# Performance work log

Hardware: AMD Instinct MI355X
Metric: run time of the kernel (lower is better)

The kernel has to match this reference:

```python
import jax, jax.numpy as jnp
import numpy as np

D = 1024          # model_dim
BD = D // 2       # bottleneck_dim
K = 64            # num_splats
B, S = 8, 2048


def setup_inputs() -> dict:
    key = jax.random.key(0)
    ks = jax.random.split(key, 12)
    sc = 0.02
    return {
        "token_embeddings": jax.random.normal(ks[0], (B, S, D), jnp.float32),
        "splat_influences": jax.random.uniform(ks[1], (B, S, K), jnp.float32),
        # encoder: Linear(D -> BD), stored [in, out]
        "enc_W": jax.random.normal(ks[2], (D, BD), jnp.float32) * sc,
        "enc_b": jnp.zeros((BD,), jnp.float32),
        # per-splat transforms: K x Linear(BD -> BD)
        "trans_W": jax.random.normal(ks[3], (K, BD, BD), jnp.float32) * sc,
        "trans_b": jnp.zeros((K, BD), jnp.float32),
        # decoder: Linear(BD -> D)
        "dec_W": jax.random.normal(ks[4], (BD, D), jnp.float32) * sc,
        "dec_b": jnp.zeros((D,), jnp.float32),
        # flow gate: Linear(D -> D) + sigmoid
        "gate_W": jax.random.normal(ks[5], (D, D), jnp.float32) * sc,
        "gate_b": jnp.zeros((D,), jnp.float32),
    }


def reference(token_embeddings, splat_influences, enc_W, enc_b,
              trans_W, trans_b, dec_W, dec_b, gate_W, gate_b):
    # gather: [B,K,S] @ [B,S,D] -> [B,K,D]
    influences_t = jnp.swapaxes(splat_influences, 1, 2)          # [B,K,S]
    gathered = jnp.einsum('bks,bsd->bkd', influences_t, token_embeddings)
    total = jnp.clip(influences_t.sum(axis=2, keepdims=True), 1e-8, None)  # [B,K,1]
    gathered = gathered / total
    # encoder (dropout inactive at eval)
    encoded = jax.nn.relu(gathered @ enc_W + enc_b)              # [B,K,BD]
    # per-splat transform as grouped matmul
    transformed = jnp.einsum('bkd,kde->bke', encoded, trans_W) + trans_b  # [B,K,BD]
    decoded = transformed @ dec_W + dec_b                        # [B,K,D]
    # scatter back to tokens: [B,S,K] @ [B,K,D]
    flow = jnp.einsum('bsk,bkd->bsd', splat_influences, decoded)
    gate = jax.nn.sigmoid(token_embeddings @ gate_W + gate_b)    # [B,S,D]
    return flow * gate
```

## Files before the change

kernel.cpp:

```cpp
#include <hip/hip_runtime.h>

#define BB 8
#define SS 2048
#define DD 1024
#define BDD 512
#define NSP 64

typedef __attribute__((ext_vector_type(8))) short bf16x8;
typedef __attribute__((ext_vector_type(4))) float f32x4;
typedef unsigned short u16;
typedef unsigned int u32;

__device__ __forceinline__ u16 f2bf(float f) {
  u32 u = __builtin_bit_cast(u32, f);
  u = u + 0x7fffu + ((u >> 16) & 1u);
  return (u16)(u >> 16);
}

__device__ __forceinline__ void gl_lds16(const void* g, void* l) {
  __builtin_amdgcn_global_load_lds((const __attribute__((address_space(1))) void*)g,
                                   (__attribute__((address_space(3))) void*)l,
                                   16, 0, 0);
}

__global__ void k_prep_tok(const float* __restrict__ tok, u16* __restrict__ tokbf,
                           u16* __restrict__ tokT) {
  __shared__ u16 tile[64][80];
  int C0 = blockIdx.x * 64;
  int R0 = blockIdx.y * 64;
  int b = R0 >> 11, s0 = R0 & 2047;
  int t = threadIdx.x;
  int lr = t >> 3, lc = (t & 7) * 8;
#pragma unroll
  for (int i = 0; i < 2; ++i) {
    int r = lr + i * 32;
    const float* src = tok + (size_t)(R0 + r) * DD + C0 + lc;
    float4 a = *(const float4*)src;
    float4 bq = *(const float4*)(src + 4);
    uint4 v;
    v.x = f2bf(a.x) | ((u32)f2bf(a.y) << 16);
    v.y = f2bf(a.z) | ((u32)f2bf(a.w) << 16);
    v.z = f2bf(bq.x) | ((u32)f2bf(bq.y) << 16);
    v.w = f2bf(bq.z) | ((u32)f2bf(bq.w) << 16);
    *(uint4*)(tokbf + (size_t)(R0 + r) * DD + C0 + lc) = v;
    *(uint4*)&tile[r][lc] = v;
  }
  __syncthreads();
  int sseg = (t & 7) * 8;
#pragma unroll
  for (int i = 0; i < 2; ++i) {
    int dcol = (t >> 3) + i * 32;
    u16 a0 = tile[sseg + 0][dcol], a1 = tile[sseg + 1][dcol];
    u16 a2 = tile[sseg + 2][dcol], a3 = tile[sseg + 3][dcol];
    u16 a4 = tile[sseg + 4][dcol], a5 = tile[sseg + 5][dcol];
    u16 a6 = tile[sseg + 6][dcol], a7 = tile[sseg + 7][dcol];
    uint4 v;
    v.x = a0 | ((u32)a1 << 16);
    v.y = a2 | ((u32)a3 << 16);
    v.z = a4 | ((u32)a5 << 16);
    v.w = a6 | ((u32)a7 << 16);
    *(uint4*)(tokT + (size_t)b * DD * SS + (size_t)(C0 + dcol) * SS + s0 + sseg) = v;
  }
}

__global__ void k_prep_infl(const float* __restrict__ infl, u16* __restrict__ inflbf,
                            u16* __restrict__ inflT, float* __restrict__ rsum) {
  __shared__ u16 tile[64][80];
  __shared__ float ps[32][64];
  int R0 = blockIdx.x * 64;
  int b = R0 >> 11, s0 = R0 & 2047;
  int st = s0 >> 6;
  int t = threadIdx.x;
  int lr = t >> 3, lc = (t & 7) * 8;
  float col[8];
#pragma unroll
  for (int j = 0; j < 8; ++j) col[j] = 0.f;
#pragma unroll
  for (int i = 0; i < 2; ++i) {
    int r = lr + i * 32;
    const float* src = infl + (size_t)(R0 + r) * NSP + lc;
    float4 a = *(const float4*)src;
    float4 bq = *(const float4*)(src + 4);
    col[0] += a.x; col[1] += a.y; col[2] += a.z; col[3] += a.w;
    col[4] += bq.x; col[5] += bq.y; col[6] += bq.z; col[7] += bq.w;
    uint4 v;
    v.x = f2bf(a.x) | ((u32)f2bf(a.y) << 16);
    v.y = f2bf(a.z) | ((u32)f2bf(a.w) << 16);
    v.z = f2bf(bq.x) | ((u32)f2bf(bq.y) << 16);
    v.w = f2bf(bq.z) | ((u32)f2bf(bq.w) << 16);
    *(uint4*)(inflbf + (size_t)(R0 + r) * NSP + lc) = v;
    *(uint4*)&tile[r][lc] = v;
  }
#pragma unroll
  for (int j = 0; j < 8; ++j) ps[lr][lc + j] = col[j];
  __syncthreads();
  if (t < 64) {
    float s = 0.f;
#pragma unroll
    for (int rr = 0; rr < 32; ++rr) s += ps[rr][t];
    rsum[((size_t)b * 32 + st) * 64 + t] = s;
  }
  int sseg = (t & 7) * 8;
#pragma unroll
  for (int i = 0; i < 2; ++i) {
    int dcol = (t >> 3) + i * 32;
    u16 a0 = tile[sseg + 0][dcol], a1 = tile[sseg + 1][dcol];
    u16 a2 = tile[sseg + 2][dcol], a3 = tile[sseg + 3][dcol];
    u16 a4 = tile[sseg + 4][dcol], a5 = tile[sseg + 5][dcol];
    u16 a6 = tile[sseg + 6][dcol], a7 = tile[sseg + 7][dcol];
    uint4 v;
    v.x = a0 | ((u32)a1 << 16);
    v.y = a2 | ((u32)a3 << 16);
    v.z = a4 | ((u32)a5 << 16);
    v.w = a6 | ((u32)a7 << 16);
    *(uint4*)(inflT + ((size_t)b * NSP + dcol) * SS + s0 + sseg) = v;
  }
}

__global__ void k_tot_fin(const float* __restrict__ rsum, float* __restrict__ rtot) {
  int t = threadIdx.x;
  float s = 0.f;
#pragma unroll
  for (int st = 0; st < 32; ++st)
    s += rsum[((size_t)(t >> 6) * 32 + st) * 64 + (t & 63)];
  rtot[t] = 1.f / fmaxf(s, 1e-8f);
}

__global__ void k_gatewt(const float* __restrict__ gw, u16* __restrict__ gwt) {
  __shared__ float tile[32][33];
  int n0 = blockIdx.x * 32, k0 = blockIdx.y * 32;
  int tx = threadIdx.x & 31, ty = threadIdx.x >> 5;
#pragma unroll
  for (int r = 0; r < 4; ++r) {
    int kr = ty + r * 8;
    tile[kr][tx] = gw[(k0 + kr) * DD + n0 + tx];
  }
  __syncthreads();
#pragma unroll
  for (int r = 0; r < 4; ++r) {
    int nc = ty + r * 8;
    gwt[(n0 + nc) * DD + k0 + tx] = f2bf(tile[tx][nc]);
  }
}

__global__ __launch_bounds__(256) void k_gather_mfma(const u16* __restrict__ inflT,
                                                     const u16* __restrict__ tokT,
                                                     float* __restrict__ pg) {
  __shared__ u16 As[64 * 64];
  __shared__ u16 Bs[64 * 64];
  int t = threadIdx.x;
  int l = t & 63, w = t >> 6;
  int wr = w >> 1, wc = w & 1;
  int n0 = blockIdx.x * 64;
  int b = blockIdx.y;
  int sq = blockIdx.z;
  int l15 = l & 15, lh = l >> 4;
  int srow = t >> 3, scol = (t & 7) * 8;

  const u16* ap = inflT + (size_t)b * NSP * SS;
  const u16* bp = tokT + (size_t)b * DD * SS;

  f32x4 acc[2][2];
#pragma unroll
  for (int i = 0; i < 2; ++i)
#pragma unroll
    for (int j = 0; j < 2; ++j) acc[i][j] = (f32x4){0.f, 0.f, 0.f, 0.f};

  for (int kt = 0; kt < 8; ++kt) {
    int k0 = sq * 512 + kt * 64;
#pragma unroll
    for (int i = 0; i < 2; ++i) {
      int row = srow + i * 32;
      gl_lds16(ap + row * SS + k0 + scol, &As[row * 64 + scol]);
      gl_lds16(bp + (n0 + row) * SS + k0 + scol, &Bs[row * 64 + scol]);
    }
    __syncthreads();
#pragma unroll
    for (int ks = 0; ks < 2; ++ks) {
      bf16x8 af[2], bfv[2];
#pragma unroll
      for (int mi = 0; mi < 2; ++mi)
        af[mi] = *(const bf16x8*)&As[(wr * 32 + mi * 16 + l15) * 64 + ks * 32 + lh * 8];
#pragma unroll
      for (int ni = 0; ni < 2; ++ni)
        bfv[ni] = *(const bf16x8*)&Bs[(wc * 32 + ni * 16 + l15) * 64 + ks * 32 + lh * 8];
#pragma unroll
      for (int mi = 0; mi < 2; ++mi)
#pragma unroll
        for (int ni = 0; ni < 2; ++ni)
          acc[mi][ni] = __builtin_amdgcn_mfma_f32_16x16x32_bf16(af[mi], bfv[ni], acc[mi][ni], 0, 0, 0);
    }
    __syncthreads();
  }

#pragma unroll
  for (int mi = 0; mi < 2; ++mi)
#pragma unroll
    for (int ni = 0; ni < 2; ++ni)
#pragma unroll
      for (int r = 0; r < 4; ++r) {
        int krow = wr * 32 + mi * 16 + lh * 4 + r;
        int dcol = n0 + wc * 32 + ni * 16 + l15;
        pg[((size_t)sq * 512 + b * NSP + krow) * DD + dcol] = acc[mi][ni][r];
      }
}

__global__ void k_enc_part(const float* __restrict__ pg, const float* __restrict__ rtot,
                           const float* __restrict__ encW, float* __restrict__ pe) {
  __shared__ float gl[8][64];
  int dq = blockIdx.x, mt = blockIdx.y;
  int m0 = mt * 8, d0 = dq * 64;
  int t = threadIdx.x;
  {
    int r = t >> 5, c = t & 31;
    float s1 = 0.f, s2 = 0.f;
#pragma unroll
    for (int q = 0; q < 4; ++q) {
      const float* qp = pg + ((size_t)q * 512 + m0 + r) * DD + d0;
      s1 += qp[c]; s2 += qp[c + 32];
    }
    float rt = rtot[m0 + r];
    gl[r][c] = s1 * rt;
    gl[r][c + 32] = s2 * rt;
  }
  __syncthreads();
  int n4 = (t & 127) * 4, mh = (t >> 7) * 4;
  float4 acc[4];
#pragma unroll
  for (int m = 0; m < 4; ++m) acc[m] = (float4){0.f, 0.f, 0.f, 0.f};
  for (int i = 0; i < 64; ++i) {
    float4 wv = *(const float4*)(encW + (d0 + i) * BDD + n4);
#pragma unroll
    for (int m = 0; m < 4; ++m) {
      float g = gl[mh + m][i];
      acc[m].x += g * wv.x; acc[m].y += g * wv.y;
      acc[m].z += g * wv.z; acc[m].w += g * wv.w;
    }
  }
#pragma unroll
  for (int m = 0; m < 4; ++m)
    *(float4*)(pe + ((size_t)dq * 512 + m0 + mh + m) * BDD + n4) = acc[m];
}

__global__ void k_trans_part(const float* __restrict__ pe, const float* __restrict__ encB,
                             const float* __restrict__ trW, float* __restrict__ pt) {
  __shared__ float el[8][32];
  int dq = blockIdx.x, ks = blockIdx.y;
  int d0 = dq * 32;
  int t = threadIdx.x;
  {
    int r = t >> 5, c = t & 31;
    int m = r * NSP + ks;
    float s = 0.f;
#pragma unroll
    for (int p = 0; p < 16; ++p)
      s += pe[((size_t)p * 512 + m) * BDD + d0 + c];
    el[r][c] = fmaxf(s + encB[d0 + c], 0.f);
  }
  __syncthreads();
  int n4 = (t & 127) * 4, mh = (t >> 7) * 4;
  float4 acc[4];
#pragma unroll
  for (int m = 0; m < 4; ++m) acc[m] = (float4){0.f, 0.f, 0.f, 0.f};
  for (int i = 0; i < 32; ++i) {
    float4 wv = *(const float4*)(trW + ((size_t)ks * BDD + d0 + i) * BDD + n4);
#pragma unroll
    for (int m = 0; m < 4; ++m) {
      float g = el[mh + m][i];
      acc[m].x += g * wv.x; acc[m].y += g * wv.y;
      acc[m].z += g * wv.z; acc[m].w += g * wv.w;
    }
  }
#pragma unroll
  for (int m = 0; m < 4; ++m)
    *(float4*)(pt + ((size_t)dq * 512 + (mh + m) * NSP + ks) * BDD + n4) = acc[m];
}

__global__ void k_dec_part(const float* __restrict__ pt, const float* __restrict__ trB,
                           const float* __restrict__ decW, float* __restrict__ pd) {
  __shared__ float tl[8][64];
  int dq = blockIdx.x, mt = blockIdx.y;
  int m0 = mt * 8, d0 = dq * 64;
  int t = threadIdx.x;
  {
    int r = t >> 5, c = t & 31;
    int m = m0 + r;
    float s1 = 0.f, s2 = 0.f;
#pragma unroll
    for (int p = 0; p < 16; ++p) {
      const float* qp = pt + ((size_t)p * 512 + m) * BDD + d0;
      s1 += qp[c]; s2 += qp[c + 32];
    }
    tl[r][c] = s1 + trB[(m & 63) * BDD + d0 + c];
    tl[r][c + 32] = s2 + trB[(m & 63) * BDD + d0 + c + 32];
  }
  __syncthreads();
  int n4 = t * 4;
  float4 acc[8];
#pragma unroll
  for (int m = 0; m < 8; ++m) acc[m] = (float4){0.f, 0.f, 0.f, 0.f};
  for (int i = 0; i < 64; ++i) {
    float4 wv = *(const float4*)(decW + (d0 + i) * DD + n4);
#pragma unroll
    for (int m = 0; m < 8; ++m) {
      float g = tl[m][i];
      acc[m].x += g * wv.x; acc[m].y += g * wv.y;
      acc[m].z += g * wv.z; acc[m].w += g * wv.w;
    }
  }
#pragma unroll
  for (int m = 0; m < 8; ++m)
    *(float4*)(pd + ((size_t)dq * 512 + m0 + m) * DD + n4) = acc[m];
}

__global__ void red_dec(const float* __restrict__ pd, const float* __restrict__ decB,
                        u16* __restrict__ decT) {
  __shared__ u16 st[64][34];
  int nt = blockIdx.x, b = blockIdx.y;
  int n0 = nt * 32;
  int t = threadIdx.x;
  int nn = t & 31, kg = t >> 5;
  float db = decB[n0 + nn];
#pragma unroll
  for (int ki = 0; ki < 8; ++ki) {
    int ks = kg * 8 + ki;
    float s = db;
#pragma unroll
    for (int p = 0; p < 8; ++p)
      s += pd[((size_t)p * 512 + b * NSP + ks) * DD + n0 + nn];
    st[ks][nn] = f2bf(s);
  }
  __syncthreads();
  int nr = t >> 3, kseg = (t & 7) * 8;
  uint4 v;
  v.x = st[kseg + 0][nr] | ((u32)st[kseg + 1][nr] << 16);
  v.y = st[kseg + 2][nr] | ((u32)st[kseg + 3][nr] << 16);
  v.z = st[kseg + 4][nr] | ((u32)st[kseg + 5][nr] << 16);
  v.w = st[kseg + 6][nr] | ((u32)st[kseg + 7][nr] << 16);
  *(uint4*)(decT + ((size_t)b * DD + n0 + nr) * NSP + kseg) = v;
}


#define STAGE_A(sl, k0, p)                                                  \
  { int e = (p)*512 + t; int row = e >> 3, csrc = ((e & 7) ^ (row & 7)) * 8; \
    gl_lds16(tokbf + (size_t)(m0 + row) * DD + (k0) + csrc, &As[sl][e * 8]); }
#define STAGE_B(sl, k0, p)                                                  \
  { int e = (p)*512 + t; int row = e >> 3, csrc = ((e & 7) ^ (row & 7)) * 8; \
    gl_lds16(gwt + (size_t)(n0 + row) * DD + (k0) + csrc, &Bs[sl][e * 8]); }

#define PHASE(sl, ks, ACC, STAGE_STMT)                                       \
  {                                                                          \
    bf16x8 af[4], bfv[4];                                                    \
    int g = (ks)*4 + lh;                                                     \
    _Pragma("unroll")                                                        \
    for (int mi = 0; mi < 4; ++mi) {                                         \
      int r = wr * 64 + mi * 16 + l15;                                       \
      af[mi] = *(const bf16x8*)&As[sl][r * 64 + (g ^ (r & 7)) * 8];          \
    }                                                                        \
    _Pragma("unroll")                                                        \
    for (int ni = 0; ni < 4; ++ni) {                                         \
      int r = wc * 64 + ni * 16 + l15;                                       \
      bfv[ni] = *(const bf16x8*)&Bs[sl][r * 64 + (g ^ (r & 7)) * 8];         \
    }                                                                        \
    STAGE_STMT;                                                              \
    __builtin_amdgcn_s_setprio(1);                                           \
    _Pragma("unroll")                                                        \
    for (int mi = 0; mi < 4; ++mi)                                           \
      _Pragma("unroll")                                                      \
      for (int ni = 0; ni < 4; ++ni)                                         \
        ACC[mi][ni] = __builtin_amdgcn_mfma_f32_16x16x32_bf16(af[mi], bfv[ni], ACC[mi][ni], 0, 0, 0); \
    __builtin_amdgcn_s_setprio(0);                                           \
  }

__global__ __launch_bounds__(512, 2) void k_out(const u16* __restrict__ tokbf,
                                                const u16* __restrict__ gwt,
                                                const u16* __restrict__ inflbf,
                                                const u16* __restrict__ decT,
                                                const float* __restrict__ gateB,
                                                float* __restrict__ outp) {
  __shared__ u16 As[2][128 * 64];
  __shared__ u16 Bs[2][256 * 64];
  int t = threadIdx.x;
  int l = t & 63, w = t >> 6;
  int wr = w >> 2, wc = w & 3;
  int m0 = blockIdx.x * 128, n0 = blockIdx.y * 256;
  int l15 = l & 15, lh = l >> 4;

  f32x4 accg[4][4];
#pragma unroll
  for (int i = 0; i < 4; ++i)
#pragma unroll
    for (int j = 0; j < 4; ++j) accg[i][j] = (f32x4){0.f, 0.f, 0.f, 0.f};

  STAGE_A(0, 0, 0); STAGE_B(0, 0, 0); STAGE_B(0, 0, 1);
  STAGE_A(0, 0, 1); STAGE_B(0, 0, 2); STAGE_B(0, 0, 3);
  asm volatile("s_waitcnt vmcnt(0)" ::: "memory");
  __builtin_amdgcn_s_barrier();

#pragma unroll 1
  for (int i = 0; i < 8; ++i) {
    int kb = i * 128 + 64;
    int kc = kb + 64;
    PHASE(0, 0, accg, { STAGE_A(1, kb, 0); STAGE_B(1, kb, 0); STAGE_B(1, kb, 1); });
    PHASE(0, 1, accg, { STAGE_A(1, kb, 1); STAGE_B(1, kb, 2); STAGE_B(1, kb, 3); });
    asm volatile("s_waitcnt vmcnt(0)" ::: "memory");
    __builtin_amdgcn_s_barrier();
    if (i < 7) {
      PHASE(1, 0, accg, { STAGE_A(0, kc, 0); STAGE_B(0, kc, 0); STAGE_B(0, kc, 1); });
      PHASE(1, 1, accg, { STAGE_A(0, kc, 1); STAGE_B(0, kc, 2); STAGE_B(0, kc, 3); });
    } else {
      PHASE(1, 0, accg, {});
      PHASE(1, 1, accg, {});
    }
    asm volatile("s_waitcnt vmcnt(0)" ::: "memory");
    __builtin_amdgcn_s_barrier();
  }

  int b = m0 >> 11;
  int s0m = m0 & 2047;
#pragma unroll
  for (int p = 0; p < 2; ++p) {
    int e = p * 512 + t;
    int row = e >> 3, csrc = ((e & 7) ^ (row & 7)) * 8;
    gl_lds16(inflbf + ((size_t)b * SS + s0m + row) * NSP + csrc, &As[0][e * 8]);
  }
#pragma unroll
  for (int p = 0; p < 4; ++p) {
    int e = p * 512 + t;
    int row = e >> 3, csrc = ((e & 7) ^ (row & 7)) * 8;
    gl_lds16(decT + ((size_t)b * DD + n0 + row) * NSP + csrc, &Bs[0][e * 8]);
  }
  asm volatile("s_waitcnt vmcnt(0)" ::: "memory");
  __builtin_amdgcn_s_barrier();

  f32x4 accf[4][4];
#pragma unroll
  for (int i = 0; i < 4; ++i)
#pragma unroll
    for (int j = 0; j < 4; ++j) accf[i][j] = (f32x4){0.f, 0.f, 0.f, 0.f};
  PHASE(0, 0, accf, {});
  PHASE(0, 1, accf, {});

  float gb[4];
#pragma unroll
  for (int ni = 0; ni < 4; ++ni) gb[ni] = gateB[n0 + wc * 64 + ni * 16 + l15];
#pragma unroll
  for (int mi = 0; mi < 4; ++mi)
#pragma unroll
    for (int ni = 0; ni < 4; ++ni)
#pragma unroll
      for (int r = 0; r < 4; ++r) {
        int mr = m0 + wr * 64 + mi * 16 + lh * 4 + r;
        int nc = n0 + wc * 64 + ni * 16 + l15;
        float z = accg[mi][ni][r] + gb[ni];
        float gate = 1.f / (1.f + __expf(-z));
        outp[(size_t)mr * DD + nc] = accf[mi][ni][r] * gate;
      }
}

extern "C" void kernel_launch(void* const* d_in, const int* in_sizes, int n_in,
                              void* d_out, int out_size, void* d_ws, size_t ws_size,
                              hipStream_t stream) {
  const float* tok = (const float*)d_in[0];
  const float* infl = (const float*)d_in[1];
  const float* encW = (const float*)d_in[2];
  const float* encB = (const float*)d_in[3];
  const float* trW = (const float*)d_in[4];
  const float* trB = (const float*)d_in[5];
  const float* decW = (const float*)d_in[6];
  const float* decB = (const float*)d_in[7];
  const float* gw = (const float*)d_in[8];
  const float* gateB = (const float*)d_in[9];
  float* outp = (float*)d_out;

  char* wsp = (char*)d_ws;
  u16* tokbf = (u16*)(wsp);
  u16* gwt = (u16*)(wsp + 33554432);
  u16* inflbf = (u16*)(wsp + 35651584);
  float* rtot = (float*)(wsp + 37748736);
  u16* decT = (u16*)(wsp + 41945088);
  u16* tokT = (u16*)(wsp + 42993664);
  float* pe = (float*)(wsp + 42993664);
  float* pt = (float*)(wsp + 42993664 + 16777216);
  u16* inflT = (u16*)(wsp + 76548096);
  float* rsum = (float*)(wsp + 78645248);
  float* scratch = (float*)(wsp + 78710784);

  k_prep_tok<<<dim3(16, 256), dim3(256), 0, stream>>>(tok, tokbf, tokT);
  k_prep_infl<<<dim3(256), dim3(256), 0, stream>>>(infl, inflbf, inflT, rsum);
  k_tot_fin<<<dim3(1), dim3(512), 0, stream>>>(rsum, rtot);
  k_gatewt<<<dim3(32, 32), dim3(256), 0, stream>>>(gw, gwt);
  k_gather_mfma<<<dim3(16, 8, 4), dim3(256), 0, stream>>>(inflT, tokT, scratch);
  k_enc_part<<<dim3(16, 64), dim3(256), 0, stream>>>(scratch, rtot, encW, pe);
  k_trans_part<<<dim3(16, 64), dim3(256), 0, stream>>>(pe, encB, trW, pt);
  k_dec_part<<<dim3(8, 64), dim3(256), 0, stream>>>(pt, trB, decW, scratch);
  red_dec<<<dim3(32, 8), dim3(256), 0, stream>>>(scratch, decB, decT);
  k_out<<<dim3(128, 4), dim3(512), 0, stream>>>(tokbf, gwt, inflbf, decT, gateB, outp);
}
```

Baseline: 173.4 us.

## Triple-buffer gate GEMM LDS tiles with partial vmcnt waits in k_out

The gate GEMM main loop in k_out moves from double to triple buffering of the A/B LDS tiles. It prefetches two k-tiles ahead and waits with vmcnt(6) instead of draining every load with vmcnt(0). Extra s_barriers are added between the fragment reads and the MFMA blocks to keep waves in lockstep. The aim is to hide global-to-LDS load latency. In exchange, LDS per block rises to about 144KB, which likely cannot fit the two blocks per CU requested by launch_bounds, and the added barriers cost sync time.

Measured after the change: 175.9 us. About the same (+1.4%).

```diff
diff --git a/kernel.cpp b/kernel.cpp
--- a/kernel.cpp
+++ b/kernel.cpp
@@ -348,7 +348,7 @@
   { int e = (p)*512 + t; int row = e >> 3, csrc = ((e & 7) ^ (row & 7)) * 8; \
     gl_lds16(gwt + (size_t)(n0 + row) * DD + (k0) + csrc, &Bs[sl][e * 8]); }
 
-#define PHASE(sl, ks, ACC, STAGE_STMT)                                       \
+#define PHASE2(sl, ks, ACC, STAGE_STMT)                                      \
   {                                                                          \
     bf16x8 af[4], bfv[4];                                                    \
     int g = (ks)*4 + lh;                                                     \
@@ -363,6 +363,7 @@
       bfv[ni] = *(const bf16x8*)&Bs[sl][r * 64 + (g ^ (r & 7)) * 8];         \
     }                                                                        \
     STAGE_STMT;                                                              \
+    __builtin_amdgcn_s_barrier();                                            \
     __builtin_amdgcn_s_setprio(1);                                           \
     _Pragma("unroll")                                                        \
     for (int mi = 0; mi < 4; ++mi)                                           \
@@ -372,14 +373,29 @@
     __builtin_amdgcn_s_setprio(0);                                           \
   }
 
+#define TILE_FULL(sl, ssl, sk, VMSTR)                                        \
+  PHASE2(sl, 0, accg, { STAGE_A(ssl, sk, 0); STAGE_A(ssl, sk, 1);            \
+                        STAGE_B(ssl, sk, 0); STAGE_B(ssl, sk, 1); });        \
+  __builtin_amdgcn_s_barrier();                                              \
+  PHASE2(sl, 1, accg, { STAGE_B(ssl, sk, 2); STAGE_B(ssl, sk, 3); });        \
+  asm volatile("s_waitcnt " VMSTR ::: "memory");                             \
+  __builtin_amdgcn_s_barrier();
+
+#define TILE_NOST(sl, VMSTR)                                                 \
+  PHASE2(sl, 0, accg, {});                                                   \
+  __builtin_amdgcn_s_barrier();                                              \
+  PHASE2(sl, 1, accg, {});                                                   \
+  asm volatile("s_waitcnt " VMSTR ::: "memory");                             \
+  __builtin_amdgcn_s_barrier();
+
 __global__ __launch_bounds__(512, 2) void k_out(const u16* __restrict__ tokbf,
                                                 const u16* __restrict__ gwt,
                                                 const u16* __restrict__ inflbf,
                                                 const u16* __restrict__ decT,
                                                 const float* __restrict__ gateB,
                                                 float* __restrict__ outp) {
-  __shared__ u16 As[2][128 * 64];
-  __shared__ u16 Bs[2][256 * 64];
+  __shared__ u16 As[3][128 * 64];
+  __shared__ u16 Bs[3][256 * 64];
   int t = threadIdx.x;
   int l = t & 63, w = t >> 6;
   int wr = w >> 2, wc = w & 3;
@@ -392,29 +408,24 @@
 #pragma unroll
     for (int j = 0; j < 4; ++j) accg[i][j] = (f32x4){0.f, 0.f, 0.f, 0.f};
 
-  STAGE_A(0, 0, 0); STAGE_B(0, 0, 0); STAGE_B(0, 0, 1);
-  STAGE_A(0, 0, 1); STAGE_B(0, 0, 2); STAGE_B(0, 0, 3);
-  asm volatile("s_waitcnt vmcnt(0)" ::: "memory");
+  STAGE_A(0, 0, 0); STAGE_A(0, 0, 1);
+  STAGE_B(0, 0, 0); STAGE_B(0, 0, 1); STAGE_B(0, 0, 2); STAGE_B(0, 0, 3);
+  STAGE_A(1, 64, 0); STAGE_A(1, 64, 1);
+  STAGE_B(1, 64, 0); STAGE_B(1, 64, 1); STAGE_B(1, 64, 2); STAGE_B(1, 64, 3);
+  asm volatile("s_waitcnt vmcnt(6)" ::: "memory");
   __builtin_amdgcn_s_barrier();
 
 #pragma unroll 1
-  for (int i = 0; i < 8; ++i) {
-    int kb = i * 128 + 64;
-    int kc = kb + 64;
-    PHASE(0, 0, accg, { STAGE_A(1, kb, 0); STAGE_B(1, kb, 0); STAGE_B(1, kb, 1); });
-    PHASE(0, 1, accg, { STAGE_A(1, kb, 1); STAGE_B(1, kb, 2); STAGE_B(1, kb, 3); });
-    asm volatile("s_waitcnt vmcnt(0)" ::: "memory");
-    __builtin_amdgcn_s_barrier();
-    if (i < 7) {
-      PHASE(1, 0, accg, { STAGE_A(0, kc, 0); STAGE_B(0, kc, 0); STAGE_B(0, kc, 1); });
-      PHASE(1, 1, accg, { STAGE_A(0, kc, 1); STAGE_B(0, kc, 2); STAGE_B(0, kc, 3); });
-    } else {
-      PHASE(1, 0, accg, {});
-      PHASE(1, 1, accg, {});
-    }
-    asm volatile("s_waitcnt vmcnt(0)" ::: "memory");
-    __builtin_amdgcn_s_barrier();
-  }
+  for (int i = 0; i < 4; ++i) {
+    int kc = i * 192;
+    TILE_FULL(0, 2, kc + 128, "vmcnt(6)");
+    TILE_FULL(1, 0, kc + 192, "vmcnt(6)");
+    TILE_FULL(2, 1, kc + 256, "vmcnt(6)");
+  }
+  TILE_FULL(0, 2, 896, "vmcnt(6)");
+  TILE_FULL(1, 0, 960, "vmcnt(6)");
+  TILE_NOST(2, "vmcnt(0)");
+  TILE_NOST(0, "vmcnt(0)");
 
   int b = m0 >> 11;
   int s0m = m0 & 2047;
@@ -438,8 +449,9 @@
   for (int i = 0; i < 4; ++i)
 #pragma unroll
     for (int j = 0; j < 4; ++j) accf[i][j] = (f32x4){0.f, 0.f, 0.f, 0.f};
-  PHASE(0, 0, accf, {});
-  PHASE(0, 1, accf, {});
+  PHASE2(0, 0, accf, {});
+  __builtin_amdgcn_s_barrier();
+  PHASE2(0, 1, accf, {});
 
   float gb[4];
 #pragma unroll
```

## Enlarge k_out tile to 256x256 with finer-grained pipelined staging and bf16 gate spill

Applied to the files above, without the earlier changes.

The fused gate-GEMM plus scatter output kernel moves from 128x256 to 256x256 tiles, so each wave holds an 8x4 accumulator grid. Staging is split into finer sub-phases with vmcnt(2) waits, so loads overlap with MFMA work more tightly. The influence/decoder tiles for the scatter GEMM are prefetched during the last gate iteration. A swizzled 1D block-to-tile mapping improves L2 locality, and the gate pre-activations are packed to bf16 to free registers for the second accumulator set. The risks are higher register pressure and LDS use at two blocks per CU, fewer blocks (256) on the device, and a bf16-rounded gate input.

Measured after the change: 189.8 us. +9.5%, slower.

```diff
diff --git a/kernel.cpp b/kernel.cpp
--- a/kernel.cpp
+++ b/kernel.cpp
@@ -341,35 +341,66 @@
 }
 
 
-#define STAGE_A(sl, k0, p)                                                  \
-  { int e = (p)*512 + t; int row = e >> 3, csrc = ((e & 7) ^ (row & 7)) * 8; \
-    gl_lds16(tokbf + (size_t)(m0 + row) * DD + (k0) + csrc, &As[sl][e * 8]); }
-#define STAGE_B(sl, k0, p)                                                  \
-  { int e = (p)*512 + t; int row = e >> 3, csrc = ((e & 7) ^ (row & 7)) * 8; \
-    gl_lds16(gwt + (size_t)(n0 + row) * DD + (k0) + csrc, &Bs[sl][e * 8]); }
-
-#define PHASE(sl, ks, ACC, STAGE_STMT)                                       \
-  {                                                                          \
-    bf16x8 af[4], bfv[4];                                                    \
-    int g = (ks)*4 + lh;                                                     \
-    _Pragma("unroll")                                                        \
-    for (int mi = 0; mi < 4; ++mi) {                                         \
-      int r = wr * 64 + mi * 16 + l15;                                       \
-      af[mi] = *(const bf16x8*)&As[sl][r * 64 + (g ^ (r & 7)) * 8];          \
-    }                                                                        \
-    _Pragma("unroll")                                                        \
-    for (int ni = 0; ni < 4; ++ni) {                                         \
-      int r = wc * 64 + ni * 16 + l15;                                       \
-      bfv[ni] = *(const bf16x8*)&Bs[sl][r * 64 + (g ^ (r & 7)) * 8];         \
-    }                                                                        \
-    STAGE_STMT;                                                              \
-    __builtin_amdgcn_s_setprio(1);                                           \
-    _Pragma("unroll")                                                        \
-    for (int mi = 0; mi < 4; ++mi)                                           \
-      _Pragma("unroll")                                                      \
-      for (int ni = 0; ni < 4; ++ni)                                         \
-        ACC[mi][ni] = __builtin_amdgcn_mfma_f32_16x16x32_bf16(af[mi], bfv[ni], ACC[mi][ni], 0, 0, 0); \
-    __builtin_amdgcn_s_setprio(0);                                           \
+#define VM2 asm volatile("s_waitcnt vmcnt(2)" ::: "memory");
+#define VM0 asm volatile("s_waitcnt vmcnt(0)" ::: "memory");
+
+#define STA(sl, k0, p)                                                        \
+  { int e = (p)*512 + t; int row = e >> 3; int cs = ((e & 7) ^ (row & 7)) * 8; \
+    gl_lds16(tokbf + (size_t)(m0 + row) * DD + (k0) + cs, &As[sl][e * 8]); }
+#define STB(sl, k0, p)                                                        \
+  { int e = (p)*512 + t; int row = e >> 3; int cs = ((e & 7) ^ (row & 7)) * 8; \
+    gl_lds16(gwt + (size_t)(n0 + row) * DD + (k0) + cs, &Bs[sl][e * 8]); }
+#define SAI(sl, p)                                                            \
+  { int e = (p)*512 + t; int row = e >> 3; int cs = ((e & 7) ^ (row & 7)) * 8; \
+    gl_lds16(inflbf + ((size_t)bb * SS + s0m + row) * NSP + cs, &As[sl][e * 8]); }
+#define SBD(sl, p)                                                            \
+  { int e = (p)*512 + t; int row = e >> 3; int cs = ((e & 7) ^ (row & 7)) * 8; \
+    gl_lds16(decT + ((size_t)bb * DD + n0 + row) * NSP + cs, &Bs[sl][e * 8]); }
+
+#define PH0(sl, CC, ACC, W, STG)                                              \
+  {                                                                           \
+    W __builtin_amdgcn_s_barrier();                                           \
+    bf16x8 af[4];                                                             \
+    _Pragma("unroll")                                                         \
+    for (int mi_ = 0; mi_ < 4; ++mi_)                                         \
+      af[mi_] = *(const bf16x8*)&As[sl][aB + mi_ * 1024 + (CC)];              \
+    _Pragma("unroll")                                                         \
+    for (int ni_ = 0; ni_ < 4; ++ni_)                                         \
+      bfv[ni_] = *(const bf16x8*)&Bs[sl][bB + ni_ * 1024 + (CC)];             \
+    STG                                                                       \
+    __builtin_amdgcn_s_setprio(1);                                            \
+    _Pragma("unroll")                                                         \
+    for (int mi_ = 0; mi_ < 4; ++mi_)                                         \
+      _Pragma("unroll")                                                       \
+      for (int ni_ = 0; ni_ < 4; ++ni_)                                       \
+        ACC[mi_][ni_] = __builtin_amdgcn_mfma_f32_16x16x32_bf16(af[mi_], bfv[ni_], ACC[mi_][ni_], 0, 0, 0); \
+    __builtin_amdgcn_s_setprio(0);                                            \
+  }
+
+#define PH1(sl, CC, ACC, W, STG)                                              \
+  {                                                                           \
+    W __builtin_amdgcn_s_barrier();                                           \
+    bf16x8 af[4];                                                             \
+    _Pragma("unroll")                                                         \
+    for (int mi_ = 0; mi_ < 4; ++mi_)                                         \
+      af[mi_] = *(const bf16x8*)&As[sl][aB + 4096 + mi_ * 1024 + (CC)];       \
+    STG                                                                       \
+    __builtin_amdgcn_s_setprio(1);                                            \
+    _Pragma("unroll")                                                         \
+    for (int mi_ = 0; mi_ < 4; ++mi_)                                         \
+      _Pragma("unroll")                                                       \
+      for (int ni_ = 0; ni_ < 4; ++ni_)                                       \
+        ACC[4 + mi_][ni_] = __builtin_amdgcn_mfma_f32_16x16x32_bf16(af[mi_], bfv[ni_], ACC[4 + mi_][ni_], 0, 0, 0); \
+    __builtin_amdgcn_s_setprio(0);                                            \
+  }
+
+#define GTILE(sl, ACC, W0, W1, S0, S1, S2, S3)                                \
+  {                                                                           \
+    bf16x8 bfv[4];                                                            \
+    PH0(sl, c0, ACC, W0, S0)                                                  \
+    PH1(sl, c0, ACC, W1, S1)                                                  \
+    PH0(sl, c1, ACC, , S2)                                                    \
+    PH1(sl, c1, ACC, , S3)                                                    \
   }
 
 __global__ __launch_bounds__(512, 2) void k_out(const u16* __restrict__ tokbf,
@@ -378,83 +409,83 @@
                                                 const u16* __restrict__ decT,
                                                 const float* __restrict__ gateB,
                                                 float* __restrict__ outp) {
-  __shared__ u16 As[2][128 * 64];
+  __shared__ u16 As[2][256 * 64];
   __shared__ u16 Bs[2][256 * 64];
   int t = threadIdx.x;
   int l = t & 63, w = t >> 6;
   int wr = w >> 2, wc = w & 3;
-  int m0 = blockIdx.x * 128, n0 = blockIdx.y * 256;
+  int bid = blockIdx.x;
+  int wg = (bid & 7) * 32 + (bid >> 3);
+  int mt = wg & 63, nt = wg >> 6;
+  int m0 = mt * 256, n0 = nt * 256;
   int l15 = l & 15, lh = l >> 4;
-
-  f32x4 accg[4][4];
-#pragma unroll
-  for (int i = 0; i < 4; ++i)
+  int x7 = l15 & 7;
+  int c0 = (lh ^ x7) * 8;
+  int c1 = ((4 + lh) ^ x7) * 8;
+  int aB = (wr * 128 + l15) * 64;
+  int bB = (wc * 64 + l15) * 64;
+  int bb = m0 >> 11;
+  int s0m = m0 & 2047;
+
+  f32x4 accg[8][4];
+#pragma unroll
+  for (int i = 0; i < 8; ++i)
 #pragma unroll
     for (int j = 0; j < 4; ++j) accg[i][j] = (f32x4){0.f, 0.f, 0.f, 0.f};
 
-  STAGE_A(0, 0, 0); STAGE_B(0, 0, 0); STAGE_B(0, 0, 1);
-  STAGE_A(0, 0, 1); STAGE_B(0, 0, 2); STAGE_B(0, 0, 3);
-  asm volatile("s_waitcnt vmcnt(0)" ::: "memory");
-  __builtin_amdgcn_s_barrier();
+  STB(0, 0, 0) STB(0, 0, 1) STB(0, 0, 2) STB(0, 0, 3)
+  STA(0, 0, 0) STA(0, 0, 2) STA(0, 0, 1) STA(0, 0, 3)
 
 #pragma unroll 1
-  for (int i = 0; i < 8; ++i) {
-    int kb = i * 128 + 64;
-    int kc = kb + 64;
-    PHASE(0, 0, accg, { STAGE_A(1, kb, 0); STAGE_B(1, kb, 0); STAGE_B(1, kb, 1); });
-    PHASE(0, 1, accg, { STAGE_A(1, kb, 1); STAGE_B(1, kb, 2); STAGE_B(1, kb, 3); });
-    asm volatile("s_waitcnt vmcnt(0)" ::: "memory");
-    __builtin_amdgcn_s_barrier();
-    if (i < 7) {
-      PHASE(1, 0, accg, { STAGE_A(0, kc, 0); STAGE_B(0, kc, 0); STAGE_B(0, kc, 1); });
-      PHASE(1, 1, accg, { STAGE_A(0, kc, 1); STAGE_B(0, kc, 2); STAGE_B(0, kc, 3); });
-    } else {
-      PHASE(1, 0, accg, {});
-      PHASE(1, 1, accg, {});
-    }
-    asm volatile("s_waitcnt vmcnt(0)" ::: "memory");
-    __builtin_amdgcn_s_barrier();
-  }
-
-  int b = m0 >> 11;
-  int s0m = m0 & 2047;
-#pragma unroll
-  for (int p = 0; p < 2; ++p) {
-    int e = p * 512 + t;
-    int row = e >> 3, csrc = ((e & 7) ^ (row & 7)) * 8;
-    gl_lds16(inflbf + ((size_t)b * SS + s0m + row) * NSP + csrc, &As[0][e * 8]);
-  }
-#pragma unroll
-  for (int p = 0; p < 4; ++p) {
-    int e = p * 512 + t;
-    int row = e >> 3, csrc = ((e & 7) ^ (row & 7)) * 8;
-    gl_lds16(decT + ((size_t)b * DD + n0 + row) * NSP + csrc, &Bs[0][e * 8]);
-  }
-  asm volatile("s_waitcnt vmcnt(0)" ::: "memory");
-  __builtin_amdgcn_s_barrier();
-
-  f32x4 accf[4][4];
-#pragma unroll
-  for (int i = 0; i < 4; ++i)
+  for (int i = 0; i < 7; ++i) {
+    int ka = i * 128 + 64;
+    int kb = ka + 64;
+    GTILE(0, accg, VM2, VM2,
+          STB(1, ka, 0) STB(1, ka, 1), STB(1, ka, 2) STB(1, ka, 3),
+          STA(1, ka, 0) STA(1, ka, 2), STA(1, ka, 1) STA(1, ka, 3))
+    GTILE(1, accg, VM2, VM2,
+          STB(0, kb, 0) STB(0, kb, 1), STB(0, kb, 2) STB(0, kb, 3),
+          STA(0, kb, 0) STA(0, kb, 2), STA(0, kb, 1) STA(0, kb, 3))
+  }
+  GTILE(0, accg, VM2, VM2,
+        STB(1, 960, 0) STB(1, 960, 1), STB(1, 960, 2) STB(1, 960, 3),
+        STA(1, 960, 0) STA(1, 960, 2), STA(1, 960, 1) STA(1, 960, 3))
+  GTILE(1, accg, VM2, VM2,
+        SBD(0, 0) SBD(0, 1), SBD(0, 2) SBD(0, 3),
+        SAI(0, 0) SAI(0, 2), SAI(0, 1) SAI(0, 3))
+
+  u32 zp[8][4][2];
+#pragma unroll
+  for (int a = 0; a < 8; ++a)
+#pragma unroll
+    for (int ni = 0; ni < 4; ++ni) {
+      zp[a][ni][0] = f2bf(accg[a][ni][0]) | ((u32)f2bf(accg[a][ni][1]) << 16);
+      zp[a][ni][1] = f2bf(accg[a][ni][2]) | ((u32)f2bf(accg[a][ni][3]) << 16);
+    }
+
+  f32x4 accf[8][4];
+#pragma unroll
+  for (int i = 0; i < 8; ++i)
 #pragma unroll
     for (int j = 0; j < 4; ++j) accf[i][j] = (f32x4){0.f, 0.f, 0.f, 0.f};
-  PHASE(0, 0, accf, {});
-  PHASE(0, 1, accf, {});
+  GTILE(0, accf, VM2, VM0, , , , )
 
   float gb[4];
 #pragma unroll
   for (int ni = 0; ni < 4; ++ni) gb[ni] = gateB[n0 + wc * 64 + ni * 16 + l15];
 #pragma unroll
-  for (int mi = 0; mi < 4; ++mi)
+  for (int a = 0; a < 8; ++a)
 #pragma unroll
     for (int ni = 0; ni < 4; ++ni)
 #pragma unroll
       for (int r = 0; r < 4; ++r) {
-        int mr = m0 + wr * 64 + mi * 16 + lh * 4 + r;
+        int mr = m0 + wr * 128 + a * 16 + lh * 4 + r;
         int nc = n0 + wc * 64 + ni * 16 + l15;
-        float z = accg[mi][ni][r] + gb[ni];
+        u32 wz = zp[a][ni][r >> 1];
+        u32 h = (r & 1) ? (wz & 0xffff0000u) : (wz << 16);
+        float z = __builtin_bit_cast(float, h) + gb[ni];
         float gate = 1.f / (1.f + __expf(-z));
-        outp[(size_t)mr * DD + nc] = accf[mi][ni][r] * gate;
+        outp[(size_t)mr * DD + nc] = accf[a][ni][r] * gate;
       }
 }
 
@@ -495,5 +526,5 @@
   k_trans_part<<<dim3(16, 64), dim3(256), 0, stream>>>(pe, encB, trW, pt);
   k_dec_part<<<dim3(8, 64), dim3(256), 0, stream>>>(pt, trB, decW, scratch);
   red_dec<<<dim3(32, 8), dim3(256), 0, stream>>>(scratch, decB, decT);
-  k_out<<<dim3(128, 4), dim3(512), 0, stream>>>(tokbf, gwt, inflbf, decT, gateB, outp);
-}
+  k_out<<<dim3(256), dim3(512), 0, stream>>>(tokbf, gwt, inflbf, decT, gateB, outp);
+}
```
